# Kernel tuning notes

Measured on AMD Instinct MI355X. Metric: run time of the kernel, lower is better.

Reference implementation:

```python
import jax, jax.numpy as jnp
import numpy as np

MARGIN = 1.0
EPS = 1e-6


def _cos(a, b):
    # Row-wise cosine similarity, matching torch.nn.CosineSimilarity semantics:
    # dot / max(||a|| * ||b||, eps)
    num = jnp.sum(a * b, axis=-1)
    den = jnp.maximum(jnp.linalg.norm(a, axis=-1) * jnp.linalg.norm(b, axis=-1), EPS)
    return num / den


def setup_inputs() -> dict:
    key = jax.random.key(0)
    k1, k2, k3 = jax.random.split(key, 3)
    B, D = 16384, 1024
    output = jax.random.normal(k1, (B, D), dtype=jnp.float32)
    target = jax.random.normal(k2, (B, D), dtype=jnp.float32)
    # offset in [0, B-1); j = (i + 1 + neg_idx) % B guarantees j != i, uniform over the rest
    neg_idx = jax.random.randint(k3, (B,), 0, B - 1, dtype=jnp.int64)
    return {"output": output, "target": target, "neg_idx": neg_idx}


def reference(output, target, neg_idx):
    B = output.shape[0]
    j = (jnp.arange(B) + 1 + neg_idx) % B  # random negative index, j != i
    t_neg = target[j]                       # gather negative label embeddings [B, D]
    hinge = jax.nn.relu(MARGIN - _cos(target, output) + _cos(t_neg, output))
    return jnp.sum(hinge) / B
```

## Files before the change

### kernel.cpp

```cpp
#include <hip/hip_runtime.h>


#define EPS 1e-6f

typedef float f4 __attribute__((ext_vector_type(4)));

#define DPP_STEP(x, ctrl, rm, bm)                                             \
    x += __int_as_float(__builtin_amdgcn_update_dpp(                          \
        0, __float_as_int(x), (ctrl), (rm), (bm), true))

__device__ __forceinline__ float dpp_wave_sum(float x) {
    DPP_STEP(x, 0x111, 0xf, 0xf);
    DPP_STEP(x, 0x112, 0xf, 0xf);
    DPP_STEP(x, 0x114, 0xf, 0xe);
    DPP_STEP(x, 0x118, 0xf, 0xc);
    DPP_STEP(x, 0x142, 0xa, 0xf);
    DPP_STEP(x, 0x143, 0xc, 0xf);
    return x;
}

struct RowBuf {
    f4 o[4], t[4], n[4];
};

__device__ __forceinline__ void issue_loads(RowBuf& rb,
                                            const float* __restrict__ outm,
                                            const float* __restrict__ tgt,
                                            int i, int j, int lane, int D) {
    const f4* o4 = (const f4*)(outm + (size_t)i * D);
    const f4* t4 = (const f4*)(tgt  + (size_t)i * D);
    const f4* n4 = (const f4*)(tgt  + (size_t)j * D);
#pragma unroll
    for (int k = 0; k < 4; ++k)
        rb.o[k] = __builtin_nontemporal_load(&o4[lane + 64 * k]);
#pragma unroll
    for (int k = 0; k < 4; ++k) rb.t[k] = t4[lane + 64 * k];
#pragma unroll
    for (int k = 0; k < 4; ++k) rb.n[k] = n4[lane + 64 * k];
}

__device__ __forceinline__ float consume(const RowBuf& rb) {
    float dto = 0.f, dno = 0.f, oo = 0.f, tt = 0.f, nn = 0.f;
#pragma unroll
    for (int k = 0; k < 4; ++k) {
        dto += rb.o[k].x*rb.t[k].x + rb.o[k].y*rb.t[k].y + rb.o[k].z*rb.t[k].z + rb.o[k].w*rb.t[k].w;
        dno += rb.o[k].x*rb.n[k].x + rb.o[k].y*rb.n[k].y + rb.o[k].z*rb.n[k].z + rb.o[k].w*rb.n[k].w;
        oo  += rb.o[k].x*rb.o[k].x + rb.o[k].y*rb.o[k].y + rb.o[k].z*rb.o[k].z + rb.o[k].w*rb.o[k].w;
        tt  += rb.t[k].x*rb.t[k].x + rb.t[k].y*rb.t[k].y + rb.t[k].z*rb.t[k].z + rb.t[k].w*rb.t[k].w;
        nn  += rb.n[k].x*rb.n[k].x + rb.n[k].y*rb.n[k].y + rb.n[k].z*rb.n[k].z + rb.n[k].w*rb.n[k].w;
    }
    dto = dpp_wave_sum(dto);
    dno = dpp_wave_sum(dno);
    oo  = dpp_wave_sum(oo);
    tt  = dpp_wave_sum(tt);
    nn  = dpp_wave_sum(nn);
    float no = sqrtf(oo);
    float h  = 1.f - dto / fmaxf(sqrtf(tt) * no, EPS)
                   + dno / fmaxf(sqrtf(nn) * no, EPS);
    return fmaxf(h, 0.f);
}

__global__ __launch_bounds__(256, 4) void hinge_cos_kernel(
    const float* __restrict__ outm,
    const float* __restrict__ tgt,
    const int*   __restrict__ negidx,
    float* __restrict__ res,
    int B, int D, float invB) {

    const int lane  = threadIdx.x & 63;
    const int wave  = threadIdx.x >> 6;
    const int wpb   = blockDim.x >> 6;
    const int gwave = blockIdx.x * wpb + wave;
    const int nwav  = gridDim.x * wpb;

    const int i0 = gwave;
    const int i1 = i0 + nwav;
    const bool v0 = i0 < B, v1 = i1 < B;

    int g0 = v0 ? negidx[i0] : 0;
    int g1 = v1 ? negidx[i1] : 0;
    int j0 = i0 + 1 + g0; if (j0 >= B) j0 -= B;
    int j1 = i1 + 1 + g1; if (j1 >= B) j1 -= B;

    float acc = 0.f;
    RowBuf bufA, bufB;

    if (v0) issue_loads(bufA, outm, tgt, i0, j0, lane, D);
    if (v1) issue_loads(bufB, outm, tgt, i1, j1, lane, D);
    if (v0) { float h = consume(bufA); if (lane == 63) acc += h; }
    if (v1) { float h = consume(bufB); if (lane == 63) acc += h; }

    __shared__ float red[4];
    if (lane == 63) red[wave] = acc;
    __syncthreads();
    if (threadIdx.x == 0) {
        float s = red[0] + red[1] + red[2] + red[3];
        atomicAdd(res, s * invB);
    }
}

extern "C" void kernel_launch(void* const* d_in, const int* in_sizes, int n_in,
                              void* d_out, int out_size, void* d_ws, size_t ws_size,
                              hipStream_t stream) {
    const float* outm   = (const float*)d_in[0];
    const float* tgt    = (const float*)d_in[1];
    const int*   negidx = (const int*)d_in[2];
    float* res = (float*)d_out;

    const int B = in_sizes[2];
    const int D = in_sizes[0] / B;

    (void)hipMemsetAsync(res, 0, sizeof(float), stream);

    const int nwav   = (B + 1) / 2;
    const int blocks = (nwav + 3) / 4;
    hinge_cos_kernel<<<blocks, 256, 0, stream>>>(outm, tgt, negidx, res, B, D,
                                                 1.0f / (float)B);
}
```

Before: 151.6 us.

## Stream rows through LDS with global_load_lds triple-buffered pipeline, four rows per wave

Each wave now handles four rows instead of two. It streams 1 KB quarter-row chunks of output, target and negative target into a three-slot per-wave LDS ring using direct global-to-LDS loads, with manual vmcnt waits and inline ds_read_b128. This keeps several loads in flight while earlier chunks are reduced, and it frees the registers the old approach spent holding whole rows. The cost is fewer waves in the grid, a 36 KB LDS footprint per block that can limit occupancy, hand-written waitcnt and asm that are fragile, and the loss of the nontemporal hint on the output loads.

```diff
diff --git a/kernel.cpp b/kernel.cpp
--- a/kernel.cpp
+++ b/kernel.cpp
@@ -1,4 +1,5 @@
 #include <hip/hip_runtime.h>
+#include <stdint.h>
 
 
 #define EPS 1e-6f
@@ -19,46 +20,69 @@
     return x;
 }
 
-struct RowBuf {
-    f4 o[4], t[4], n[4];
-};
-
-__device__ __forceinline__ void issue_loads(RowBuf& rb,
-                                            const float* __restrict__ outm,
-                                            const float* __restrict__ tgt,
-                                            int i, int j, int lane, int D) {
-    const f4* o4 = (const f4*)(outm + (size_t)i * D);
-    const f4* t4 = (const f4*)(tgt  + (size_t)i * D);
-    const f4* n4 = (const f4*)(tgt  + (size_t)j * D);
-#pragma unroll
-    for (int k = 0; k < 4; ++k)
-        rb.o[k] = __builtin_nontemporal_load(&o4[lane + 64 * k]);
-#pragma unroll
-    for (int k = 0; k < 4; ++k) rb.t[k] = t4[lane + 64 * k];
-#pragma unroll
-    for (int k = 0; k < 4; ++k) rb.n[k] = n4[lane + 64 * k];
-}
-
-__device__ __forceinline__ float consume(const RowBuf& rb) {
-    float dto = 0.f, dno = 0.f, oo = 0.f, tt = 0.f, nn = 0.f;
-#pragma unroll
-    for (int k = 0; k < 4; ++k) {
-        dto += rb.o[k].x*rb.t[k].x + rb.o[k].y*rb.t[k].y + rb.o[k].z*rb.t[k].z + rb.o[k].w*rb.t[k].w;
-        dno += rb.o[k].x*rb.n[k].x + rb.o[k].y*rb.n[k].y + rb.o[k].z*rb.n[k].z + rb.o[k].w*rb.n[k].w;
-        oo  += rb.o[k].x*rb.o[k].x + rb.o[k].y*rb.o[k].y + rb.o[k].z*rb.o[k].z + rb.o[k].w*rb.o[k].w;
-        tt  += rb.t[k].x*rb.t[k].x + rb.t[k].y*rb.t[k].y + rb.t[k].z*rb.t[k].z + rb.t[k].w*rb.t[k].w;
-        nn  += rb.n[k].x*rb.n[k].x + rb.n[k].y*rb.n[k].y + rb.n[k].z*rb.n[k].z + rb.n[k].w*rb.n[k].w;
-    }
-    dto = dpp_wave_sum(dto);
-    dno = dpp_wave_sum(dno);
-    oo  = dpp_wave_sum(oo);
-    tt  = dpp_wave_sum(tt);
-    nn  = dpp_wave_sum(nn);
-    float no = sqrtf(oo);
-    float h  = 1.f - dto / fmaxf(sqrtf(tt) * no, EPS)
-                   + dno / fmaxf(sqrtf(nn) * no, EPS);
-    return fmaxf(h, 0.f);
-}
+__device__ __forceinline__ void gload16(const float* g, char* l) {
+    __builtin_amdgcn_global_load_lds(
+        (__attribute__((address_space(1))) void*)g,
+        (__attribute__((address_space(3))) void*)l, 16, 0, 0);
+}
+
+__device__ __forceinline__ uint32_t lds_addr(void* p) {
+    return (uint32_t)(uintptr_t)(__attribute__((address_space(3))) char*)p;
+}
+
+#define WAITV(n)                                                              \
+    asm volatile("s_waitcnt vmcnt(" #n ")" ::: "memory");                     \
+    __builtin_amdgcn_sched_barrier(0)
+
+#define DSR(slot)                                                             \
+    asm volatile("ds_read_b128 %0, %3 offset:0\n\t"                           \
+                 "ds_read_b128 %1, %3 offset:1024\n\t"                        \
+                 "ds_read_b128 %2, %3 offset:2048\n\t"                        \
+                 "s_waitcnt lgkmcnt(0)"                                       \
+                 : "=&v"(vo), "=&v"(vt), "=&v"(vn)                            \
+                 : "v"(va##slot))
+
+#define ISSUE3(slot, r, q)                                                    \
+    gload16(gO##r + (q)*256 + lane4, wslot##slot);                            \
+    gload16(gT##r + (q)*256 + lane4, wslot##slot + 1024);                     \
+    gload16(gN##r + (q)*256 + lane4, wslot##slot + 2048)
+
+#define ACCQ()                                                                \
+    dto += vo.x*vt.x + vo.y*vt.y + vo.z*vt.z + vo.w*vt.w;                     \
+    dno += vo.x*vn.x + vo.y*vn.y + vo.z*vn.z + vo.w*vn.w;                     \
+    oo  += vo.x*vo.x + vo.y*vo.y + vo.z*vo.z + vo.w*vo.w;                     \
+    tt  += vt.x*vt.x + vt.y*vt.y + vt.z*vt.z + vt.w*vt.w;                     \
+    nn  += vn.x*vn.x + vn.y*vn.y + vn.z*vn.z + vn.w*vn.w
+
+#define STEP_I(W, slot, r, q, nslot, nr, nq)                                  \
+    do {                                                                      \
+        WAITV(W);                                                             \
+        f4 vo, vt, vn;                                                        \
+        DSR(slot);                                                            \
+        ISSUE3(nslot, nr, nq);                                                \
+        ACCQ();                                                               \
+    } while (0)
+
+#define STEP_N(W, slot, r, q)                                                 \
+    do {                                                                      \
+        WAITV(W);                                                             \
+        f4 vo, vt, vn;                                                        \
+        DSR(slot);                                                            \
+        ACCQ();                                                               \
+    } while (0)
+
+#define ROWINIT() dto = dno = oo = tt = nn = 0.f
+
+#define FIN()                                                                 \
+    do {                                                                      \
+        float d1 = dpp_wave_sum(dto), d2 = dpp_wave_sum(dno);                 \
+        float s1 = dpp_wave_sum(oo);                                          \
+        float s2 = dpp_wave_sum(tt), s3 = dpp_wave_sum(nn);                   \
+        float no_ = sqrtf(s1);                                                \
+        float h = 1.f - d1 / fmaxf(sqrtf(s2) * no_, EPS)                      \
+                      + d2 / fmaxf(sqrtf(s3) * no_, EPS);                     \
+        if (lane == 63) acc += fmaxf(h, 0.f);                                 \
+    } while (0)
 
 __global__ __launch_bounds__(256, 4) void hinge_cos_kernel(
     const float* __restrict__ outm,
@@ -69,28 +93,102 @@
 
     const int lane  = threadIdx.x & 63;
     const int wave  = threadIdx.x >> 6;
-    const int wpb   = blockDim.x >> 6;
-    const int gwave = blockIdx.x * wpb + wave;
-    const int nwav  = gridDim.x * wpb;
+    const int gwave = blockIdx.x * 4 + wave;
+    const int nwav  = gridDim.x * 4;
 
     const int i0 = gwave;
     const int i1 = i0 + nwav;
-    const bool v0 = i0 < B, v1 = i1 < B;
-
-    int g0 = v0 ? negidx[i0] : 0;
-    int g1 = v1 ? negidx[i1] : 0;
-    int j0 = i0 + 1 + g0; if (j0 >= B) j0 -= B;
-    int j1 = i1 + 1 + g1; if (j1 >= B) j1 -= B;
+    const int i2 = i1 + nwav;
+    const int i3 = i2 + nwav;
+
+    __shared__ char smem[4 * 3 * 3072];
+    __shared__ float red[4];
 
     float acc = 0.f;
-    RowBuf bufA, bufB;
-
-    if (v0) issue_loads(bufA, outm, tgt, i0, j0, lane, D);
-    if (v1) issue_loads(bufB, outm, tgt, i1, j1, lane, D);
-    if (v0) { float h = consume(bufA); if (lane == 63) acc += h; }
-    if (v1) { float h = consume(bufB); if (lane == 63) acc += h; }
-
-    __shared__ float red[4];
+
+    if (i3 < B) {
+        int g0 = negidx[i0], g1 = negidx[i1], g2 = negidx[i2], g3 = negidx[i3];
+        int j0 = i0 + 1 + g0; if (j0 >= B) j0 -= B;
+        int j1 = i1 + 1 + g1; if (j1 >= B) j1 -= B;
+        int j2 = i2 + 1 + g2; if (j2 >= B) j2 -= B;
+        int j3 = i3 + 1 + g3; if (j3 >= B) j3 -= B;
+
+        const float* gO0 = outm + (size_t)i0 * D;
+        const float* gT0 = tgt  + (size_t)i0 * D;
+        const float* gN0 = tgt  + (size_t)j0 * D;
+        const float* gO1 = outm + (size_t)i1 * D;
+        const float* gT1 = tgt  + (size_t)i1 * D;
+        const float* gN1 = tgt  + (size_t)j1 * D;
+        const float* gO2 = outm + (size_t)i2 * D;
+        const float* gT2 = tgt  + (size_t)i2 * D;
+        const float* gN2 = tgt  + (size_t)j2 * D;
+        const float* gO3 = outm + (size_t)i3 * D;
+        const float* gT3 = tgt  + (size_t)i3 * D;
+        const float* gN3 = tgt  + (size_t)j3 * D;
+
+        const int lane4 = lane * 4;
+
+        char* wb     = &smem[wave * 9216];
+        char* wslot0 = wb;
+        char* wslot1 = wb + 3072;
+        char* wslot2 = wb + 6144;
+        const uint32_t vabase = lds_addr(wb) + (uint32_t)(lane * 16);
+        const uint32_t va0 = vabase;
+        const uint32_t va1 = vabase + 3072;
+        const uint32_t va2 = vabase + 6144;
+
+        float dto, dno, oo, tt, nn;
+
+        ISSUE3(0, 0, 0);
+        ISSUE3(1, 0, 1);
+        ISSUE3(2, 0, 2);
+
+        ROWINIT();
+        STEP_I(6, 0, 0, 0, 0, 0, 3);
+        STEP_I(6, 1, 0, 1, 1, 1, 0);
+        STEP_I(6, 2, 0, 2, 2, 1, 1);
+        STEP_I(6, 0, 0, 3, 0, 1, 2);
+        FIN();
+        ROWINIT();
+        STEP_I(6, 1, 1, 0, 1, 1, 3);
+        STEP_I(6, 2, 1, 1, 2, 2, 0);
+        STEP_I(6, 0, 1, 2, 0, 2, 1);
+        STEP_I(6, 1, 1, 3, 1, 2, 2);
+        FIN();
+        ROWINIT();
+        STEP_I(6, 2, 2, 0, 2, 2, 3);
+        STEP_I(6, 0, 2, 1, 0, 3, 0);
+        STEP_I(6, 1, 2, 2, 1, 3, 1);
+        STEP_I(6, 2, 2, 3, 2, 3, 2);
+        FIN();
+        ROWINIT();
+        STEP_I(6, 0, 3, 0, 0, 3, 3);
+        STEP_N(6, 1, 3, 1);
+        STEP_N(3, 2, 3, 2);
+        STEP_N(0, 0, 3, 3);
+        FIN();
+    } else {
+        int idx[4] = {i0, i1, i2, i3};
+        for (int r = 0; r < 4; ++r) {
+            int i = idx[r];
+            if (i >= B) break;
+            int g = negidx[i];
+            int j = i + 1 + g; if (j >= B) j -= B;
+            const f4* o4 = (const f4*)(outm + (size_t)i * D);
+            const f4* t4 = (const f4*)(tgt  + (size_t)i * D);
+            const f4* n4 = (const f4*)(tgt  + (size_t)j * D);
+            float dto = 0.f, dno = 0.f, oo = 0.f, tt = 0.f, nn = 0.f;
+#pragma unroll
+            for (int k = 0; k < 4; ++k) {
+                f4 vo = o4[lane + 64*k], vt = t4[lane + 64*k], vn = n4[lane + 64*k];
+                ACCQ();
+            }
+            float acc_local;
+            (void)acc_local;
+            FIN();
+        }
+    }
+
     if (lane == 63) red[wave] = acc;
     __syncthreads();
     if (threadIdx.x == 0) {
@@ -112,7 +210,7 @@
 
     (void)hipMemsetAsync(res, 0, sizeof(float), stream);
 
-    const int nwav   = (B + 1) / 2;
+    const int nwav   = (B + 3) / 4;
     const int blocks = (nwav + 3) / 4;
     hinge_cos_kernel<<<blocks, 256, 0, stream>>>(outm, tgt, negidx, res, B, D,
                                                  1.0f / (float)B);
```

After: 145.6 us. 3.9% less time.
